# Kernel tuning notes

Measured on AMD Instinct MI355X. Metric: run time of the kernel, lower is better.

## Reference

```python
import jax, jax.numpy as jnp
import numpy as np

N_CELL, N_DRUG = 8192, 4096
E_CELL, E_DRUG = 262144, 131072
D_OUT = 128


def setup_inputs() -> dict:
    key = jax.random.key(0)
    ks = jax.random.split(key, 8)
    cell_feat = jax.random.normal(ks[0], (N_CELL, N_CELL), dtype=jnp.float32)
    drug_feat = jax.random.normal(ks[1], (N_DRUG, N_DRUG), dtype=jnp.float32)
    cell_edge = jax.random.randint(ks[2], (2, E_CELL), 0, N_CELL, dtype=jnp.int64)
    drug_edge = jax.random.randint(ks[3], (2, E_DRUG), 0, N_DRUG, dtype=jnp.int64)
    W_cell = jax.random.normal(ks[4], (N_CELL, D_OUT), dtype=jnp.float32) * 0.02
    W_drug = jax.random.normal(ks[5], (N_DRUG, D_OUT), dtype=jnp.float32) * 0.02
    b_cell = jnp.zeros((D_OUT,), dtype=jnp.float32)
    b_drug = jnp.zeros((D_OUT,), dtype=jnp.float32)
    return {"cell_feat": cell_feat, "cell_edge": cell_edge, "W_cell": W_cell,
            "b_cell": b_cell, "drug_feat": drug_feat, "drug_edge": drug_edge,
            "W_drug": W_drug, "b_drug": b_drug}


def _gcn_conv(x, edge, W, b):
    """PyG GCNConv with edge_weight = x[row, col] (as in GEncoder.forward),
    add_self_loops=True, symmetric normalization."""
    N = x.shape[0]
    row, col = edge[0], edge[1]
    ew = x[row, col]                                  # [E] gathered edge weights
    loop = jnp.arange(N)
    row = jnp.concatenate([row, loop])                # [E+N] self-loops appended
    col = jnp.concatenate([col, loop])
    ew = jnp.concatenate([ew, jnp.ones((N,), x.dtype)])
    deg = jax.ops.segment_sum(ew, col, num_segments=N)
    dinv = jnp.where(deg > 0, jax.lax.rsqrt(jnp.maximum(deg, 1e-30)), 0.0)
    norm = dinv[row] * ew * dinv[col]                 # [E+N]
    h = x @ W                                         # [N, D_OUT]
    msg = norm[:, None] * h[row]                      # gather + scale
    out = jax.ops.segment_sum(msg, col, num_segments=N) + b
    return jax.nn.relu(out)


def reference(cell_feat, cell_edge, W_cell, b_cell, drug_feat, drug_edge, W_drug, b_drug):
    cell_gcn = _gcn_conv(cell_feat, cell_edge, W_cell, b_cell)
    drug_gcn = _gcn_conv(drug_feat, drug_edge, W_drug, b_drug)
    return (cell_gcn, drug_gcn)
```

## Files before the change

### kernel.cpp

```cpp
#include <hip/hip_runtime.h>
#include <stdint.h>

#define N_CELL 8192
#define N_DRUG 4096
#define E_CELL 262144
#define E_DRUG 131072
#define DOUT   128

typedef float f32x4 __attribute__((ext_vector_type(4)));
typedef short s16x8 __attribute__((ext_vector_type(8)));

#define OFF_DEG_C   0u
#define OFF_DEG_D   8192u
#define OFF_CNT_C   12288u
#define OFF_CNT_D   20480u
#define OFF_CUR_C   24576u
#define OFF_CUR_D   32768u
#define OFF_START_C 36864u
#define OFF_START_D 45312u
#define OFF_EW_C    49664u
#define OFF_EW_D    311808u
#define OFF_SROW_C  442880u
#define OFF_SROW_D  705024u
#define OFF_SCOEF_C 836096u
#define OFF_SCOEF_D 1098240u
#define OFF_H_C     1229312u
#define OFF_H_D     2277888u
#define OFF_END     2802176u
#define WT_C_BYTE   (OFF_END * 4u)
#define WT_D_BYTE   (WT_C_BYTE + 128u * 8192u * 2u)
#define PART_C_BYTE 14354432u
#define PART_D_BYTE 31131648u
#define PART_END    35325952u

__device__ __forceinline__ unsigned short f2bf(float f) {
    union { float f; uint32_t u; } v; v.f = f;
    uint32_t u = v.u + 0x7fffu + ((v.u >> 16) & 1u);
    return (unsigned short)(u >> 16);
}

__device__ __forceinline__ s16x8 pack8(float4 x, float4 y) {
    union { float4 f; uint32_t u[4]; } a, b;
    a.f = x; b.f = y;
    union { uint32_t u[4]; s16x8 v; } r;
    r.u[0] = __builtin_amdgcn_perm(a.u[1] + 0x8000u, a.u[0] + 0x8000u, 0x07060302u);
    r.u[1] = __builtin_amdgcn_perm(a.u[3] + 0x8000u, a.u[2] + 0x8000u, 0x07060302u);
    r.u[2] = __builtin_amdgcn_perm(b.u[1] + 0x8000u, b.u[0] + 0x8000u, 0x07060302u);
    r.u[3] = __builtin_amdgcn_perm(b.u[3] + 0x8000u, b.u[2] + 0x8000u, 0x07060302u);
    return r.v;
}

__global__ __launch_bounds__(256) void k_prep(const float* __restrict__ Wc, const float* __restrict__ Wd,
                                              unsigned short* __restrict__ wtc, unsigned short* __restrict__ wtd,
                                              float* __restrict__ ws) {
    int bid = blockIdx.x, t = threadIdx.x;
    if (bid < 144) {
        int i = bid * 256 + t;
        ws[i] = (i < 12288) ? 1.0f : 0.0f;
        return;
    }
    if (bid < 1680) {
        size_t i = (size_t)(bid - 144) * 256 + t;
        ((float4*)(ws + OFF_H_C))[i] = make_float4(0.f, 0.f, 0.f, 0.f);
        return;
    }
    int tile = bid - 1680;
    const float* W; unsigned short* wt; int K;
    if (tile < 1024) { W = Wc; wt = wtc; K = N_CELL; }
    else             { W = Wd; wt = wtd; K = N_DRUG; tile -= 1024; }
    int tk = tile >> 2, tc = tile & 3;
    __shared__ float tl[32][33];
    int c = t & 31, r8 = t >> 5;
#pragma unroll
    for (int p = 0; p < 4; ++p) {
        int row = r8 + p * 8;
        tl[row][c] = W[(size_t)(tk * 32 + row) * DOUT + tc * 32 + c];
    }
    __syncthreads();
#pragma unroll
    for (int p = 0; p < 4; ++p) {
        int c2 = r8 + p * 8;
        wt[(size_t)(tc * 32 + c2) * K + tk * 32 + c] = f2bf(tl[c][c2]);
    }
}

__global__ __launch_bounds__(256) void k_edge(const float* __restrict__ xc, const int* __restrict__ ec,
                                              const float* __restrict__ xd, const int* __restrict__ ed,
                                              float* __restrict__ ws) {
    int i = blockIdx.x * 256 + threadIdx.x;
    const float* x; const int* edges; float* ew; float* deg; int* cnt; int N, E, idx;
    if (i < E_CELL) {
        idx = i; x = xc; edges = ec; N = N_CELL; E = E_CELL;
        ew = ws + OFF_EW_C; deg = ws + OFF_DEG_C; cnt = (int*)(ws + OFF_CNT_C);
    } else {
        idx = i - E_CELL; if (idx >= E_DRUG) return;
        x = xd; edges = ed; N = N_DRUG; E = E_DRUG;
        ew = ws + OFF_EW_D; deg = ws + OFF_DEG_D; cnt = (int*)(ws + OFF_CNT_D);
    }
    int r = edges[idx], c = edges[E + idx];
    float w = x[(size_t)r * N + c];
    ew[idx] = w;
    unsafeAtomicAdd(&deg[c], w);
    atomicAdd(&cnt[c], 1);
}

__global__ __launch_bounds__(256) void k_scan2(float* ws) {
    int bid = blockIdx.x, t = threadIdx.x;
    if (bid < 48) {
        int i = bid * 256 + t;
        float d = ws[i];
        ws[i] = d > 0.f ? rsqrtf(fmaxf(d, 1e-30f)) : 0.f;
        return;
    }
    const int* cnt; int* start; int N, chunk;
    if (bid == 48) { cnt = (const int*)(ws + OFF_CNT_C); start = (int*)(ws + OFF_START_C); N = N_CELL; chunk = 32; }
    else           { cnt = (const int*)(ws + OFF_CNT_D); start = (int*)(ws + OFF_START_D); N = N_DRUG; chunk = 16; }
    __shared__ int sums[256];
    int base = t * chunk;
    int s = 0;
    for (int j = 0; j < chunk; ++j) s += cnt[base + j];
    sums[t] = s; __syncthreads();
    for (int off = 1; off < 256; off <<= 1) {
        int v = (t >= off) ? sums[t - off] : 0;
        __syncthreads();
        sums[t] += v;
        __syncthreads();
    }
    int run = sums[t] - s;
    for (int j = 0; j < chunk; ++j) { start[base + j] = run; run += cnt[base + j]; }
    if (t == 255) start[N] = run;
}

__global__ __launch_bounds__(256) void k_fill(const int* __restrict__ ec, const int* __restrict__ ed,
                                              float* __restrict__ ws) {
    int i = blockIdx.x * 256 + threadIdx.x;
    const int* edges; const float* ew; const float* dinv; const int* start;
    int* cur; int* srow; float* scoef; int E, idx;
    if (i < E_CELL) {
        idx = i; edges = ec; E = E_CELL;
        ew = ws + OFF_EW_C; dinv = ws + OFF_DEG_C; start = (const int*)(ws + OFF_START_C);
        cur = (int*)(ws + OFF_CUR_C); srow = (int*)(ws + OFF_SROW_C); scoef = ws + OFF_SCOEF_C;
    } else {
        idx = i - E_CELL; if (idx >= E_DRUG) return;
        edges = ed; E = E_DRUG;
        ew = ws + OFF_EW_D; dinv = ws + OFF_DEG_D; start = (const int*)(ws + OFF_START_D);
        cur = (int*)(ws + OFF_CUR_D); srow = (int*)(ws + OFF_SROW_D); scoef = ws + OFF_SCOEF_D;
    }
    int r = edges[idx], c = edges[E + idx];
    float coef = dinv[r] * ew[idx] * dinv[c];
    int slot = start[c] + atomicAdd(&cur[c], 1);
    srow[slot] = r;
    scoef[slot] = coef;
}

__global__ __launch_bounds__(256, 3) void k_gemm(const float* __restrict__ xc, const float* __restrict__ xd,
                                                 const unsigned short* __restrict__ wtc,
                                                 const unsigned short* __restrict__ wtd,
                                                 float* __restrict__ ws,
                                                 float* __restrict__ partC, float* __restrict__ partD,
                                                 int usePart) {
    int bid = blockIdx.x, t = threadIdx.x;
    const float* x; const unsigned short* wt; float* hp; float* part; int K, mt, ch; size_t pstride;
    if (bid < 1024) {
        x = xc; wt = wtc; hp = ws + OFF_H_C; part = partC; K = N_CELL;
        mt = bid >> 2; ch = bid & 3; pstride = (size_t)N_CELL * DOUT;
    } else {
        int b = bid - 1024; x = xd; wt = wtd; hp = ws + OFF_H_D; part = partD; K = N_DRUG;
        mt = b >> 1; ch = b & 1; pstride = (size_t)N_DRUG * DOUT;
    }
    int k0 = ch * 2048;

    __shared__ alignas(16) unsigned short As[2][32][136];
    int lane = t & 63, wv = t >> 6;
    int l15 = lane & 15, l4 = lane >> 4;

    f32x4 acc00 = {}, acc01 = {}, acc10 = {}, acc11 = {};

    int srow = t >> 3, sseg = t & 7;
    const float* abase = x + (size_t)(mt * 32 + srow) * K + k0 + sseg * 16;
    const unsigned short* bb  = wt + (size_t)(wv * 32 + l15) * K + k0 + l4 * 8;
    const unsigned short* bb1 = bb + (size_t)16 * K;

    float4 X0, X1, X2, X3;
    s16x8 BA0, BA1, BA2, BA3, BA4, BA5, BA6, BA7;
    s16x8 BB0, BB1, BB2, BB3, BB4, BB5, BB6, BB7;

#define LOADA(IT) { const float4* _p = (const float4*)(abase + (size_t)(IT) * 128); \
                    X0 = _p[0]; X1 = _p[1]; X2 = _p[2]; X3 = _p[3]; }
#define WRITEA(BUF) { *(s16x8*)&As[BUF][srow][sseg * 16]     = pack8(X0, X1); \
                      *(s16x8*)&As[BUF][srow][sseg * 16 + 8] = pack8(X2, X3); }
#define BLOADM(P0,P1,P2,P3,P4,P5,P6,P7, IT) { \
    P0 = *(const s16x8*)(bb  + (size_t)(IT) * 128); \
    P1 = *(const s16x8*)(bb  + (size_t)(IT) * 128 + 32); \
    P2 = *(const s16x8*)(bb  + (size_t)(IT) * 128 + 64); \
    P3 = *(const s16x8*)(bb  + (size_t)(IT) * 128 + 96); \
    P4 = *(const s16x8*)(bb1 + (size_t)(IT) * 128); \
    P5 = *(const s16x8*)(bb1 + (size_t)(IT) * 128 + 32); \
    P6 = *(const s16x8*)(bb1 + (size_t)(IT) * 128 + 64); \
    P7 = *(const s16x8*)(bb1 + (size_t)(IT) * 128 + 96); }
#define COMPUTEM(BUF, B0,B1,B2,B3,B4,B5,B6,B7) { \
    { s16x8 a0 = *(const s16x8*)&As[BUF][l15][l4 * 8]; \
      s16x8 a1 = *(const s16x8*)&As[BUF][16 + l15][l4 * 8]; \
      acc00 = __builtin_amdgcn_mfma_f32_16x16x32_bf16(a0, B0, acc00, 0, 0, 0); \
      acc01 = __builtin_amdgcn_mfma_f32_16x16x32_bf16(a0, B4, acc01, 0, 0, 0); \
      acc10 = __builtin_amdgcn_mfma_f32_16x16x32_bf16(a1, B0, acc10, 0, 0, 0); \
      acc11 = __builtin_amdgcn_mfma_f32_16x16x32_bf16(a1, B4, acc11, 0, 0, 0); } \
    { s16x8 a0 = *(const s16x8*)&As[BUF][l15][32 + l4 * 8]; \
      s16x8 a1 = *(const s16x8*)&As[BUF][16 + l15][32 + l4 * 8]; \
      acc00 = __builtin_amdgcn_mfma_f32_16x16x32_bf16(a0, B1, acc00, 0, 0, 0); \
      acc01 = __builtin_amdgcn_mfma_f32_16x16x32_bf16(a0, B5, acc01, 0, 0, 0); \
      acc10 = __builtin_amdgcn_mfma_f32_16x16x32_bf16(a1, B1, acc10, 0, 0, 0); \
      acc11 = __builtin_amdgcn_mfma_f32_16x16x32_bf16(a1, B5, acc11, 0, 0, 0); } \
    { s16x8 a0 = *(const s16x8*)&As[BUF][l15][64 + l4 * 8]; \
      s16x8 a1 = *(const s16x8*)&As[BUF][16 + l15][64 + l4 * 8]; \
      acc00 = __builtin_amdgcn_mfma_f32_16x16x32_bf16(a0, B2, acc00, 0, 0, 0); \
      acc01 = __builtin_amdgcn_mfma_f32_16x16x32_bf16(a0, B6, acc01, 0, 0, 0); \
      acc10 = __builtin_amdgcn_mfma_f32_16x16x32_bf16(a1, B2, acc10, 0, 0, 0); \
      acc11 = __builtin_amdgcn_mfma_f32_16x16x32_bf16(a1, B6, acc11, 0, 0, 0); } \
    { s16x8 a0 = *(const s16x8*)&As[BUF][l15][96 + l4 * 8]; \
      s16x8 a1 = *(const s16x8*)&As[BUF][16 + l15][96 + l4 * 8]; \
      acc00 = __builtin_amdgcn_mfma_f32_16x16x32_bf16(a0, B3, acc00, 0, 0, 0); \
      acc01 = __builtin_amdgcn_mfma_f32_16x16x32_bf16(a0, B7, acc01, 0, 0, 0); \
      acc10 = __builtin_amdgcn_mfma_f32_16x16x32_bf16(a1, B3, acc10, 0, 0, 0); \
      acc11 = __builtin_amdgcn_mfma_f32_16x16x32_bf16(a1, B7, acc11, 0, 0, 0); } }

    LOADA(0);
    WRITEA(0);
    LOADA(1);
    BLOADM(BA0,BA1,BA2,BA3,BA4,BA5,BA6,BA7, 0);
    __syncthreads();

#pragma unroll 1
    for (int it2 = 0; it2 < 8; ++it2) {
        int itE = it2 * 2, itO = itE + 1;
        BLOADM(BB0,BB1,BB2,BB3,BB4,BB5,BB6,BB7, itO);
        WRITEA(itO & 1);
        if (itE < 14) LOADA(itE + 2);
        COMPUTEM(itE & 1, BA0,BA1,BA2,BA3,BA4,BA5,BA6,BA7);
        __syncthreads();
        if (itO < 15) {
            BLOADM(BA0,BA1,BA2,BA3,BA4,BA5,BA6,BA7, itO + 1);
            WRITEA((itO + 1) & 1);
            if (itO < 14) LOADA(itO + 2);
        }
        COMPUTEM(itO & 1, BB0,BB1,BB2,BB3,BB4,BB5,BB6,BB7);
        __syncthreads();
    }
#undef LOADA
#undef WRITEA
#undef BLOADM
#undef COMPUTEM
    if (usePart) {
        float* dst = part + (size_t)ch * pstride;
#pragma unroll
        for (int m = 0; m < 2; ++m)
#pragma unroll
            for (int n = 0; n < 2; ++n) {
                f32x4 a = (m == 0) ? (n == 0 ? acc00 : acc01) : (n == 0 ? acc10 : acc11);
                int col = wv * 32 + n * 16 + l15;
                int row = mt * 32 + m * 16 + l4 * 4;
#pragma unroll
                for (int j = 0; j < 4; ++j)
                    dst[(size_t)(row + j) * DOUT + col] = a[j];
            }
    } else {
#pragma unroll
        for (int m = 0; m < 2; ++m)
#pragma unroll
            for (int n = 0; n < 2; ++n) {
                f32x4 a = (m == 0) ? (n == 0 ? acc00 : acc01) : (n == 0 ? acc10 : acc11);
                int col = wv * 32 + n * 16 + l15;
                int row = mt * 32 + m * 16 + l4 * 4;
#pragma unroll
                for (int j = 0; j < 4; ++j)
                    unsafeAtomicAdd(&hp[(size_t)(row + j) * DOUT + col], a[j]);
            }
    }
}

__global__ __launch_bounds__(256) void k_reduce(const float* __restrict__ partC,
                                                const float* __restrict__ partD,
                                                float* __restrict__ ws) {
    int bid = blockIdx.x, t = threadIdx.x;
    if (bid < 1024) {
        size_t i = (size_t)bid * 256 + t;
        const f32x4* p = (const f32x4*)partC;
        f32x4 s = p[i] + p[i + 262144] + p[i + 2 * 262144] + p[i + 3 * 262144];
        ((f32x4*)(ws + OFF_H_C))[i] = s;
    } else {
        size_t i = (size_t)(bid - 1024) * 256 + t;
        const f32x4* p = (const f32x4*)partD;
        f32x4 s = p[i] + p[i + 131072];
        ((f32x4*)(ws + OFF_H_D))[i] = s;
    }
}

__global__ __launch_bounds__(256) void k_gather(const float* __restrict__ ws,
                                                const float* __restrict__ bc, const float* __restrict__ bd,
                                                float* __restrict__ out) {
    int wv = threadIdx.x >> 6, lane = threadIdx.x & 63;
    int g = blockIdx.x * 4 + wv;
    const float* h; const int* srow; const float* scoef; const int* start; const float* dinv;
    const float* bvec; float* outp; int node;
    if (g < N_CELL) {
        node = g; h = ws + OFF_H_C; srow = (const int*)(ws + OFF_SROW_C); scoef = ws + OFF_SCOEF_C;
        start = (const int*)(ws + OFF_START_C); dinv = ws + OFF_DEG_C; bvec = bc; outp = out;
    } else {
        node = g - N_CELL; if (node >= N_DRUG) return;
        h = ws + OFF_H_D; srow = (const int*)(ws + OFF_SROW_D); scoef = ws + OFF_SCOEF_D;
        start = (const int*)(ws + OFF_START_D); dinv = ws + OFF_DEG_D; bvec = bd;
        outp = out + (size_t)N_CELL * DOUT;
    }
    float di = dinv[node], sc = di * di;
    float2 v = ((const float2*)(h + (size_t)node * DOUT))[lane];
    float ax = sc * v.x, ay = sc * v.y;
    int s0 = start[node], s1 = start[node + 1];
    int e = s0;
    for (; e + 3 < s1; e += 4) {
        int r0 = srow[e];     float c0 = scoef[e];
        int r1 = srow[e + 1]; float c1 = scoef[e + 1];
        int r2 = srow[e + 2]; float c2 = scoef[e + 2];
        int r3 = srow[e + 3]; float c3 = scoef[e + 3];
        float2 u0 = ((const float2*)(h + (size_t)r0 * DOUT))[lane];
        float2 u1 = ((const float2*)(h + (size_t)r1 * DOUT))[lane];
        float2 u2 = ((const float2*)(h + (size_t)r2 * DOUT))[lane];
        float2 u3 = ((const float2*)(h + (size_t)r3 * DOUT))[lane];
        ax += c0 * u0.x + c1 * u1.x + c2 * u2.x + c3 * u3.x;
        ay += c0 * u0.y + c1 * u1.y + c2 * u2.y + c3 * u3.y;
    }
    for (; e < s1; ++e) {
        int r = srow[e]; float cf = scoef[e];
        float2 u = ((const float2*)(h + (size_t)r * DOUT))[lane];
        ax += cf * u.x; ay += cf * u.y;
    }
    float2 bb = ((const float2*)bvec)[lane];
    ax = fmaxf(ax + bb.x, 0.f);
    ay = fmaxf(ay + bb.y, 0.f);
    float2 o; o.x = ax; o.y = ay;
    ((float2*)outp)[(size_t)node * 64 + lane] = o;
}

extern "C" void kernel_launch(void* const* d_in, const int* in_sizes, int n_in,
                              void* d_out, int out_size, void* d_ws, size_t ws_size,
                              hipStream_t stream) {
    const float* cell_feat = (const float*)d_in[0];
    const int*   cell_edge = (const int*)d_in[1];
    const float* W_cell    = (const float*)d_in[2];
    const float* b_cell    = (const float*)d_in[3];
    const float* drug_feat = (const float*)d_in[4];
    const int*   drug_edge = (const int*)d_in[5];
    const float* W_drug    = (const float*)d_in[6];
    const float* b_drug    = (const float*)d_in[7];
    float* out = (float*)d_out;
    float* ws  = (float*)d_ws;
    unsigned short* wtc = (unsigned short*)((char*)d_ws + WT_C_BYTE);
    unsigned short* wtd = (unsigned short*)((char*)d_ws + WT_D_BYTE);
    float* partC = (float*)((char*)d_ws + PART_C_BYTE);
    float* partD = (float*)((char*)d_ws + PART_D_BYTE);
    int usePart = (ws_size >= (size_t)PART_END) ? 1 : 0;

    k_prep<<<3216, 256, 0, stream>>>(W_cell, W_drug, wtc, wtd, ws);
    k_edge<<<(E_CELL + E_DRUG) / 256, 256, 0, stream>>>(cell_feat, cell_edge, drug_feat, drug_edge, ws);
    k_scan2<<<50, 256, 0, stream>>>(ws);
    k_fill<<<1536, 256, 0, stream>>>(cell_edge, drug_edge, ws);
    k_gemm<<<1280, 256, 0, stream>>>(cell_feat, drug_feat, wtc, wtd, ws, partC, partD, usePart);
    if (usePart) k_reduce<<<1536, 256, 0, stream>>>(partC, partD, ws);
    k_gather<<<3072, 256, 0, stream>>>(ws, b_cell, b_drug, out);
}
```

Before: 228.2 us.

## Pre-cast feature matrices to bf16 in a separate pass before GEMM

```diff
diff --git a/kernel.cpp b/kernel.cpp
--- a/kernel.cpp
+++ b/kernel.cpp
@@ -32,6 +32,9 @@
 #define PART_C_BYTE 14354432u
 #define PART_D_BYTE 31131648u
 #define PART_END    35325952u
+#define XB_C_BYTE   35325952u
+#define XB_D_BYTE   169543680u
+#define XB_END      203098112u
 
 __device__ __forceinline__ unsigned short f2bf(float f) {
     union { float f; uint32_t u; } v; v.f = f;
@@ -81,6 +84,21 @@
     for (int p = 0; p < 4; ++p) {
         int c2 = r8 + p * 8;
         wt[(size_t)(tc * 32 + c2) * K + tk * 32 + c] = f2bf(tl[c][c2]);
+    }
+}
+
+__global__ __launch_bounds__(256) void k_cast(const float* __restrict__ xc, const float* __restrict__ xd,
+                                              unsigned short* __restrict__ xbC,
+                                              unsigned short* __restrict__ xbD) {
+    const size_t nC = (size_t)N_CELL * N_CELL / 8;
+    const size_t nD = (size_t)N_DRUG * N_DRUG / 8;
+    size_t stride = (size_t)gridDim.x * 256;
+    for (size_t i = (size_t)blockIdx.x * 256 + threadIdx.x; i < nC + nD; i += stride) {
+        const float4* src; unsigned short* dst; size_t j;
+        if (i < nC) { src = (const float4*)xc; dst = xbC; j = i; }
+        else        { src = (const float4*)xd; dst = xbD; j = i - nC; }
+        float4 a = src[2 * j], b = src[2 * j + 1];
+        *(s16x8*)(dst + j * 8) = pack8(a, b);
     }
 }
 
@@ -153,19 +171,18 @@
     scoef[slot] = coef;
 }
 
-__global__ __launch_bounds__(256, 3) void k_gemm(const float* __restrict__ xc, const float* __restrict__ xd,
-                                                 const unsigned short* __restrict__ wtc,
-                                                 const unsigned short* __restrict__ wtd,
-                                                 float* __restrict__ ws,
-                                                 float* __restrict__ partC, float* __restrict__ partD,
-                                                 int usePart) {
+__global__ __launch_bounds__(256, 4) void k_gemm_b(const unsigned short* __restrict__ xbC,
+                                                   const unsigned short* __restrict__ xbD,
+                                                   const unsigned short* __restrict__ wtc,
+                                                   const unsigned short* __restrict__ wtd,
+                                                   float* __restrict__ partC, float* __restrict__ partD) {
     int bid = blockIdx.x, t = threadIdx.x;
-    const float* x; const unsigned short* wt; float* hp; float* part; int K, mt, ch; size_t pstride;
+    const unsigned short* xb; const unsigned short* wt; float* part; int K, mt, ch; size_t pstride;
     if (bid < 1024) {
-        x = xc; wt = wtc; hp = ws + OFF_H_C; part = partC; K = N_CELL;
+        xb = xbC; wt = wtc; part = partC; K = N_CELL;
         mt = bid >> 2; ch = bid & 3; pstride = (size_t)N_CELL * DOUT;
     } else {
-        int b = bid - 1024; x = xd; wt = wtd; hp = ws + OFF_H_D; part = partD; K = N_DRUG;
+        int b = bid - 1024; xb = xbD; wt = wtd; part = partD; K = N_DRUG;
         mt = b >> 1; ch = b & 1; pstride = (size_t)N_DRUG * DOUT;
     }
     int k0 = ch * 2048;
@@ -177,18 +194,18 @@
     f32x4 acc00 = {}, acc01 = {}, acc10 = {}, acc11 = {};
 
     int srow = t >> 3, sseg = t & 7;
-    const float* abase = x + (size_t)(mt * 32 + srow) * K + k0 + sseg * 16;
+    const unsigned short* abase = xb + (size_t)(mt * 32 + srow) * K + k0 + sseg * 16;
     const unsigned short* bb  = wt + (size_t)(wv * 32 + l15) * K + k0 + l4 * 8;
     const unsigned short* bb1 = bb + (size_t)16 * K;
 
-    float4 X0, X1, X2, X3;
+    s16x8 X0, X1;
     s16x8 BA0, BA1, BA2, BA3, BA4, BA5, BA6, BA7;
     s16x8 BB0, BB1, BB2, BB3, BB4, BB5, BB6, BB7;
 
-#define LOADA(IT) { const float4* _p = (const float4*)(abase + (size_t)(IT) * 128); \
-                    X0 = _p[0]; X1 = _p[1]; X2 = _p[2]; X3 = _p[3]; }
-#define WRITEA(BUF) { *(s16x8*)&As[BUF][srow][sseg * 16]     = pack8(X0, X1); \
-                      *(s16x8*)&As[BUF][srow][sseg * 16 + 8] = pack8(X2, X3); }
+#define LOADA(IT) { X0 = *(const s16x8*)(abase + (size_t)(IT) * 128); \
+                    X1 = *(const s16x8*)(abase + (size_t)(IT) * 128 + 8); }
+#define WRITEA(BUF) { *(s16x8*)&As[BUF][srow][sseg * 16]     = X0; \
+                      *(s16x8*)&As[BUF][srow][sseg * 16 + 8] = X1; }
 #define BLOADM(P0,P1,P2,P3,P4,P5,P6,P7, IT) { \
     P0 = *(const s16x8*)(bb  + (size_t)(IT) * 128); \
     P1 = *(const s16x8*)(bb  + (size_t)(IT) * 128 + 32); \
@@ -250,32 +267,78 @@
 #undef WRITEA
 #undef BLOADM
 #undef COMPUTEM
-    if (usePart) {
-        float* dst = part + (size_t)ch * pstride;
-#pragma unroll
-        for (int m = 0; m < 2; ++m)
-#pragma unroll
-            for (int n = 0; n < 2; ++n) {
-                f32x4 a = (m == 0) ? (n == 0 ? acc00 : acc01) : (n == 0 ? acc10 : acc11);
-                int col = wv * 32 + n * 16 + l15;
-                int row = mt * 32 + m * 16 + l4 * 4;
-#pragma unroll
-                for (int j = 0; j < 4; ++j)
-                    dst[(size_t)(row + j) * DOUT + col] = a[j];
+    float* dst = part + (size_t)ch * pstride;
+#pragma unroll
+    for (int m = 0; m < 2; ++m)
+#pragma unroll
+        for (int n = 0; n < 2; ++n) {
+            f32x4 a = (m == 0) ? (n == 0 ? acc00 : acc01) : (n == 0 ? acc10 : acc11);
+            int col = wv * 32 + n * 16 + l15;
+            int row = mt * 32 + m * 16 + l4 * 4;
+#pragma unroll
+            for (int j = 0; j < 4; ++j)
+                dst[(size_t)(row + j) * DOUT + col] = a[j];
+        }
+}
+
+__global__ __launch_bounds__(256, 3) void k_gemm_f(const float* __restrict__ xc, const float* __restrict__ xd,
+                                                   const unsigned short* __restrict__ wtc,
+                                                   const unsigned short* __restrict__ wtd,
+                                                   float* __restrict__ ws,
+                                                   float* __restrict__ partC, float* __restrict__ partD,
+                                                   int usePart) {
+    int bid = blockIdx.x, t = threadIdx.x;
+    const float* x; const unsigned short* wt; float* hp; float* part; int K, mt, ch; size_t pstride;
+    if (bid < 1024) {
+        x = xc; wt = wtc; hp = ws + OFF_H_C; part = partC; K = N_CELL;
+        mt = bid >> 2; ch = bid & 3; pstride = (size_t)N_CELL * DOUT;
+    } else {
+        int b = bid - 1024; x = xd; wt = wtd; hp = ws + OFF_H_D; part = partD; K = N_DRUG;
+        mt = b >> 1; ch = b & 1; pstride = (size_t)N_DRUG * DOUT;
+    }
+    int k0 = ch * 2048;
+    __shared__ alignas(16) unsigned short As[2][32][136];
+    int lane = t & 63, wv = t >> 6;
+    int l15 = lane & 15, l4 = lane >> 4;
+    f32x4 acc00 = {}, acc01 = {}, acc10 = {}, acc11 = {};
+    int srow = t >> 3, sseg = t & 7;
+    const float* abase = x + (size_t)(mt * 32 + srow) * K + k0 + sseg * 16;
+    const unsigned short* bb  = wt + (size_t)(wv * 32 + l15) * K + k0 + l4 * 8;
+    const unsigned short* bb1 = bb + (size_t)16 * K;
+    float4 X0, X1, X2, X3;
+#pragma unroll 1
+    for (int it = 0; it < 16; ++it) {
+        const float4* p = (const float4*)(abase + (size_t)it * 128);
+        X0 = p[0]; X1 = p[1]; X2 = p[2]; X3 = p[3];
+        *(s16x8*)&As[it & 1][srow][sseg * 16]     = pack8(X0, X1);
+        *(s16x8*)&As[it & 1][srow][sseg * 16 + 8] = pack8(X2, X3);
+        __syncthreads();
+#pragma unroll
+        for (int ks = 0; ks < 4; ++ks) {
+            s16x8 b0 = *(const s16x8*)(bb  + (size_t)it * 128 + ks * 32);
+            s16x8 b1 = *(const s16x8*)(bb1 + (size_t)it * 128 + ks * 32);
+            s16x8 a0 = *(const s16x8*)&As[it & 1][l15][ks * 32 + l4 * 8];
+            s16x8 a1 = *(const s16x8*)&As[it & 1][16 + l15][ks * 32 + l4 * 8];
+            acc00 = __builtin_amdgcn_mfma_f32_16x16x32_bf16(a0, b0, acc00, 0, 0, 0);
+            acc01 = __builtin_amdgcn_mfma_f32_16x16x32_bf16(a0, b1, acc01, 0, 0, 0);
+            acc10 = __builtin_amdgcn_mfma_f32_16x16x32_bf16(a1, b0, acc10, 0, 0, 0);
+            acc11 = __builtin_amdgcn_mfma_f32_16x16x32_bf16(a1, b1, acc11, 0, 0, 0);
+        }
+        __syncthreads();
+    }
+#pragma unroll
+    for (int m = 0; m < 2; ++m)
+#pragma unroll
+        for (int n = 0; n < 2; ++n) {
+            f32x4 a = (m == 0) ? (n == 0 ? acc00 : acc01) : (n == 0 ? acc10 : acc11);
+            int col = wv * 32 + n * 16 + l15;
+            int row = mt * 32 + m * 16 + l4 * 4;
+#pragma unroll
+            for (int j = 0; j < 4; ++j) {
+                if (usePart) part[(size_t)ch * pstride + (size_t)(row + j) * DOUT + col] = a[j];
+                else unsafeAtomicAdd(&hp[(size_t)(row + j) * DOUT + col], a[j]);
             }
-    } else {
-#pragma unroll
-        for (int m = 0; m < 2; ++m)
-#pragma unroll
-            for (int n = 0; n < 2; ++n) {
-                f32x4 a = (m == 0) ? (n == 0 ? acc00 : acc01) : (n == 0 ? acc10 : acc11);
-                int col = wv * 32 + n * 16 + l15;
-                int row = mt * 32 + m * 16 + l4 * 4;
-#pragma unroll
-                for (int j = 0; j < 4; ++j)
-                    unsafeAtomicAdd(&hp[(size_t)(row + j) * DOUT + col], a[j]);
-            }
-    }
+        }
 }
 
 __global__ __launch_bounds__(256) void k_reduce(const float* __restrict__ partC,
@@ -357,13 +420,22 @@
     unsigned short* wtd = (unsigned short*)((char*)d_ws + WT_D_BYTE);
     float* partC = (float*)((char*)d_ws + PART_C_BYTE);
     float* partD = (float*)((char*)d_ws + PART_D_BYTE);
+    unsigned short* xbC = (unsigned short*)((char*)d_ws + XB_C_BYTE);
+    unsigned short* xbD = (unsigned short*)((char*)d_ws + XB_D_BYTE);
+    int useCast = (ws_size >= (size_t)XB_END) ? 1 : 0;
     int usePart = (ws_size >= (size_t)PART_END) ? 1 : 0;
 
     k_prep<<<3216, 256, 0, stream>>>(W_cell, W_drug, wtc, wtd, ws);
     k_edge<<<(E_CELL + E_DRUG) / 256, 256, 0, stream>>>(cell_feat, cell_edge, drug_feat, drug_edge, ws);
     k_scan2<<<50, 256, 0, stream>>>(ws);
     k_fill<<<1536, 256, 0, stream>>>(cell_edge, drug_edge, ws);
-    k_gemm<<<1280, 256, 0, stream>>>(cell_feat, drug_feat, wtc, wtd, ws, partC, partD, usePart);
-    if (usePart) k_reduce<<<1536, 256, 0, stream>>>(partC, partD, ws);
+    if (useCast) {
+        k_cast<<<2048, 256, 0, stream>>>(cell_feat, drug_feat, xbC, xbD);
+        k_gemm_b<<<1280, 256, 0, stream>>>(xbC, xbD, wtc, wtd, partC, partD);
+        k_reduce<<<1536, 256, 0, stream>>>(partC, partD, ws);
+    } else {
+        k_gemm_f<<<1280, 256, 0, stream>>>(cell_feat, drug_feat, wtc, wtd, ws, partC, partD, usePart);
+        if (usePart) k_reduce<<<1536, 256, 0, stream>>>(partC, partD, ws);
+    }
     k_gather<<<3072, 256, 0, stream>>>(ws, b_cell, b_drug, out);
 }
```

Result: slower. 296.5 us (+29.9%).
